# Kernel tuning notes

Measured on AMD Instinct MI355X. Metric: run time of the kernel, lower is better.

The kernel has to match this reference:

```python
import jax, jax.numpy as jnp
import numpy as np

B, T, C = 4, 2048, 1024
H, DH = 16, 64  # num_heads, head_size; H*DH == C


def setup_inputs() -> dict:
    key = jax.random.key(0)
    ks = jax.random.split(key, 6)
    s = C ** -0.5
    x = jax.random.normal(ks[0], (B, T, C), dtype=jnp.float32)
    # per-head projection weights, stacked: [H, C, DH]
    Wq = jax.random.normal(ks[1], (H, C, DH), dtype=jnp.float32) * s
    Wk = jax.random.normal(ks[2], (H, C, DH), dtype=jnp.float32) * s
    Wv = jax.random.normal(ks[3], (H, C, DH), dtype=jnp.float32) * s
    # output projection (with bias, as nn.Linear default)
    Wo = jax.random.normal(ks[4], (C, C), dtype=jnp.float32) * s
    bo = jax.random.normal(ks[5], (C,), dtype=jnp.float32) * 0.01
    return {"x": x, "Wq": Wq, "Wk": Wk, "Wv": Wv, "Wo": Wo, "bo": bo}


def reference(x, Wq, Wk, Wv, Wo, bo):
    Bv, Tv, Cv = x.shape
    scale = DH ** -0.5
    # project to per-head q/k/v: [B, H, T, DH]
    q = jnp.einsum('btc,hcd->bhtd', x, Wq)
    k = jnp.einsum('btc,hcd->bhtd', x, Wk)
    v = jnp.einsum('btc,hcd->bhtd', x, Wv)
    # scaled scores [B, H, T, T] with causal mask
    scores = jnp.einsum('bhtd,bhsd->bhts', q, k) * scale
    causal = jnp.tril(jnp.ones((Tv, Tv), dtype=bool))
    scores = jnp.where(causal, scores, -jnp.inf)
    wei = jax.nn.softmax(scores, axis=-1)
    out = jnp.einsum('bhts,bhsd->bhtd', wei, v)
    # concat heads: [B, T, H*DH] == [B, T, C]
    out = out.transpose(0, 2, 1, 3).reshape(Bv, Tv, Cv)
    return out @ Wo.T + bo
```

## Files before the change

kernel.cpp:

```cpp
#include <hip/hip_runtime.h>
#include <stdint.h>

typedef unsigned short u16;
typedef __attribute__((ext_vector_type(8))) short short8;
typedef __attribute__((ext_vector_type(4))) float floatx4;

#define MFMA_BF16 __builtin_amdgcn_mfma_f32_16x16x32_bf16

#define BB 4
#define TT 2048
#define CC 1024
#define HH 16
#define DH 64
#define MM (BB * TT)
#define NQKV (3 * CC)

#define SOFTMAX_OFF 23.083120654223414f

__device__ __forceinline__ u16 f2bf(float f) {
  union { float f; uint32_t u; } un;
  un.f = f;
  uint32_t u = un.u;
  u += 0x7fffu + ((u >> 16) & 1u);
  return (u16)(u >> 16);
}

__device__ __forceinline__ uint32_t pk2(float a, float b) {
  return (uint32_t)f2bf(a) | ((uint32_t)f2bf(b) << 16);
}

__device__ __forceinline__ void gload_lds16(const u16* g, u16* l) {
  __builtin_amdgcn_global_load_lds(
      (const __attribute__((address_space(1))) unsigned int*)g,
      (__attribute__((address_space(3))) unsigned int*)l, 16, 0, 0);
}

__global__ __launch_bounds__(256) void convert_kernel(
    const float* __restrict__ x, const float* __restrict__ Wq,
    const float* __restrict__ Wk, const float* __restrict__ Wv,
    const float* __restrict__ Wo, u16* __restrict__ xb,
    u16* __restrict__ Wt, u16* __restrict__ Wob) {
  __shared__ float T[32][33];
  int bid = blockIdx.x, tid = threadIdx.x;
  if (bid < 8192) {
    int i = (bid * 256 + tid) * 4;
    float4 f = *(const float4*)(x + i);
    uint2 o = {pk2(f.x, f.y), pk2(f.z, f.w)};
    *(uint2*)(xb + i) = o;
  } else if (bid < 8192 + 3072) {
    int tb = bid - 8192;
    int sec = tb >> 10, rem = tb & 1023;
    int h = rem >> 6, sub = rem & 63, ct = sub >> 1, dt = sub & 1;
    const float* W = (sec == 0) ? Wq : (sec == 1) ? Wk : Wv;
    int tx = tid & 31, ty = tid >> 5;
#pragma unroll
    for (int p = 0; p < 4; ++p)
      T[ty + 8 * p][tx] =
          W[((size_t)h * CC + ct * 32 + ty + 8 * p) * DH + dt * 32 + tx];
    __syncthreads();
#pragma unroll
    for (int p = 0; p < 4; ++p) {
      int n = sec * 1024 + h * 64 + dt * 32 + ty + 8 * p;
      Wt[(size_t)n * CC + ct * 32 + tx] = f2bf(T[tx][ty + 8 * p]);
    }
  } else {
    int i = ((bid - 11264) * 256 + tid) * 4;
    float4 f = *(const float4*)(Wo + i);
    uint2 o = {pk2(f.x, f.y), pk2(f.z, f.w)};
    *(uint2*)(Wob + i) = o;
  }
}

template <int MODE>
__global__ __launch_bounds__(256) void gemm_bt(
    const u16* __restrict__ A, const u16* __restrict__ Bt, int M, int N, int K,
    u16* __restrict__ qout, u16* __restrict__ kout, u16* __restrict__ vout,
    float* __restrict__ out, const float* __restrict__ bias) {
  __shared__ u16 As[128][64];
  __shared__ u16 Bs[128][64];
  int tid = threadIdx.x;
  int lane = tid & 63, w = tid >> 6;
  int wm = w >> 1, wn = w & 1;
  int g = lane >> 4, c = lane & 15;
  int m0 = blockIdx.y * 128, n0 = blockIdx.x * 128;

  floatx4 acc[4][4];
#pragma unroll
  for (int i = 0; i < 4; ++i)
#pragma unroll
    for (int j = 0; j < 4; ++j) acc[i][j] = (floatx4){0.f, 0.f, 0.f, 0.f};

  int srow = 32 * w + (lane >> 3);
  int scol = (lane & 7) * 8;
  const u16* Ag = A + (size_t)(m0 + srow) * K + scol;
  const u16* Bg = Bt + (size_t)(n0 + srow) * K + scol;
  u16* AsB = &As[32 * w][0];
  u16* BsB = &Bs[32 * w][0];

  for (int k0 = 0; k0 < K; k0 += 64) {
    __syncthreads();
#pragma unroll
    for (int j = 0; j < 4; ++j)
      gload_lds16(Ag + k0 + (size_t)j * 8 * K, AsB + j * 512);
#pragma unroll
    for (int j = 0; j < 4; ++j)
      gload_lds16(Bg + k0 + (size_t)j * 8 * K, BsB + j * 512);
    __syncthreads();
#pragma unroll
    for (int kc = 0; kc < 2; ++kc) {
      short8 af[4], bfv[4];
#pragma unroll
      for (int mt = 0; mt < 4; ++mt)
        af[mt] = *(const short8*)(&As[wm * 64 + mt * 16 + c][kc * 32 + g * 8]);
#pragma unroll
      for (int nt = 0; nt < 4; ++nt)
        bfv[nt] = *(const short8*)(&Bs[wn * 64 + nt * 16 + c][kc * 32 + g * 8]);
#pragma unroll
      for (int mt = 0; mt < 4; ++mt)
#pragma unroll
        for (int nt = 0; nt < 4; ++nt)
          acc[mt][nt] = MFMA_BF16(af[mt], bfv[nt], acc[mt][nt], 0, 0, 0);
    }
  }

#pragma unroll
  for (int mt = 0; mt < 4; ++mt) {
#pragma unroll
    for (int nt = 0; nt < 4; ++nt) {
#pragma unroll
      for (int r = 0; r < 4; ++r) {
        int m = m0 + wm * 64 + mt * 16 + g * 4 + r;
        int n = n0 + wn * 64 + nt * 16 + c;
        float v = acc[mt][nt][r];
        if (MODE == 0) {
          int b = m >> 11, t = m & 2047;
          int sec = n >> 10, h = (n >> 6) & 15, d = n & 63;
          size_t idx = (((size_t)(b * HH + h)) * TT + t) * DH + d;
          if (sec == 0)
            qout[idx] = f2bf(v * 0.18033688011112042f);
          else if (sec == 1)
            kout[idx] = f2bf(v);
          else
            vout[idx] = f2bf(v);
        } else {
          out[(size_t)m * N + n] = v + bias[n];
        }
      }
    }
  }
}

__global__ __launch_bounds__(256, 4) void flash_attn(
    const u16* __restrict__ q, const u16* __restrict__ k,
    const u16* __restrict__ v, u16* __restrict__ O) {
  __shared__ u16 Ks[64][72];
  __shared__ u16 Vs[64][72];
  __shared__ u16 Ps[4][32][72];

  int tid = threadIdx.x;
  int lane = tid & 63, w = tid >> 6;
  int g = lane >> 4, c = lane & 15;

  int id = blockIdx.y * 16 + blockIdx.x;
  int bh = id >> 4;
  int x = id & 15;
  int t0 = (((id >> 8) & 1) ? x : 15 - x) * 128;

  const u16* qb = q + (size_t)bh * TT * DH;
  const u16* kb = k + (size_t)bh * TT * DH;
  const u16* vb = v + (size_t)bh * TT * DH;

  short8 qf[2][2];
#pragma unroll
  for (int mt = 0; mt < 2; ++mt) {
    int qrow = t0 + w * 32 + mt * 16 + c;
#pragma unroll
    for (int kc = 0; kc < 2; ++kc)
      qf[mt][kc] = *(const short8*)(qb + (size_t)qrow * DH + kc * 32 + g * 8);
  }

  floatx4 oacc[2][4];
#pragma unroll
  for (int mt = 0; mt < 2; ++mt)
#pragma unroll
    for (int nt = 0; nt < 4; ++nt) oacc[mt][nt] = (floatx4){0.f, 0.f, 0.f, 0.f};
  float lsum[2][4];
#pragma unroll
  for (int mt = 0; mt < 2; ++mt)
#pragma unroll
    for (int r = 0; r < 4; ++r) lsum[mt][r] = 0.f;

  int srow = tid >> 2, scol = (tid & 3) * 16;
  const u16* kbase = kb + (size_t)srow * DH + scol;
  const u16* vbase = vb + (size_t)srow * DH + scol;

  uint4 kr0 = *(const uint4*)(kbase);
  uint4 kr1 = *(const uint4*)(kbase + 8);
  uint4 vr0 = *(const uint4*)(vbase);
  uint4 vr1 = *(const uint4*)(vbase + 8);

  int niter = (t0 >> 6) + 2;
  int nfull = t0 >> 6;
  int wmax = t0 + w * 32 + 31;
  for (int it = 0; it < niter; ++it) {
    int s0 = it << 6;
    __syncthreads();
    *(uint4*)(&Ks[srow][scol]) = kr0;
    *(uint4*)(&Ks[srow][scol + 8]) = kr1;
    {
      const u16* pv0 = (const u16*)&vr0;
      const u16* pv1 = (const u16*)&vr1;
#pragma unroll
      for (int j = 0; j < 8; ++j) {
        Vs[scol + j][srow] = pv0[j];
        Vs[scol + 8 + j][srow] = pv1[j];
      }
    }
    __syncthreads();
    if (it + 1 < niter) {
      size_t off = (size_t)((it + 1) << 6) * DH;
      kr0 = *(const uint4*)(kbase + off);
      kr1 = *(const uint4*)(kbase + off + 8);
      vr0 = *(const uint4*)(vbase + off);
      vr1 = *(const uint4*)(vbase + off + 8);
    }
    if (s0 > wmax) continue;
    bool masked = (it >= nfull);

    floatx4 z[2][4];
#pragma unroll
    for (int mt = 0; mt < 2; ++mt)
#pragma unroll
      for (int n = 0; n < 4; ++n) z[mt][n] = (floatx4){0.f, 0.f, 0.f, 0.f};
#pragma unroll
    for (int kc = 0; kc < 2; ++kc)
#pragma unroll
      for (int n = 0; n < 4; ++n) {
        short8 kf = *(const short8*)(&Ks[n * 16 + c][kc * 32 + g * 8]);
        z[0][n] = MFMA_BF16(qf[0][kc], kf, z[0][n], 0, 0, 0);
        z[1][n] = MFMA_BF16(qf[1][kc], kf, z[1][n], 0, 0, 0);
      }

#pragma unroll
    for (int mt = 0; mt < 2; ++mt) {
      int qr = t0 + w * 32 + mt * 16 + g * 4;
#pragma unroll
      for (int r = 0; r < 4; ++r) {
        float p0 = exp2f(z[mt][0][r] - SOFTMAX_OFF);
        float p1 = exp2f(z[mt][1][r] - SOFTMAX_OFF);
        float p2 = exp2f(z[mt][2][r] - SOFTMAX_OFF);
        float p3 = exp2f(z[mt][3][r] - SOFTMAX_OFF);
        if (masked) {
          if (s0 + c > qr + r) p0 = 0.f;
          if (s0 + 16 + c > qr + r) p1 = 0.f;
          if (s0 + 32 + c > qr + r) p2 = 0.f;
          if (s0 + 48 + c > qr + r) p3 = 0.f;
        }
        lsum[mt][r] += (p0 + p1) + (p2 + p3);
        u16* pr = &Ps[w][mt * 16 + g * 4 + r][c];
        pr[0] = f2bf(p0);
        pr[16] = f2bf(p1);
        pr[32] = f2bf(p2);
        pr[48] = f2bf(p3);
      }
    }

#pragma unroll
    for (int kc = 0; kc < 2; ++kc) {
      short8 pf0 = *(const short8*)(&Ps[w][c][kc * 32 + g * 8]);
      short8 pf1 = *(const short8*)(&Ps[w][16 + c][kc * 32 + g * 8]);
#pragma unroll
      for (int nt = 0; nt < 4; ++nt) {
        short8 vf = *(const short8*)(&Vs[nt * 16 + c][kc * 32 + g * 8]);
        oacc[0][nt] = MFMA_BF16(pf0, vf, oacc[0][nt], 0, 0, 0);
        oacc[1][nt] = MFMA_BF16(pf1, vf, oacc[1][nt], 0, 0, 0);
      }
    }
  }

  int b = bh >> 4, h = bh & 15;
#pragma unroll
  for (int mt = 0; mt < 2; ++mt) {
#pragma unroll
    for (int r = 0; r < 4; ++r) {
      float l = lsum[mt][r];
      l += __shfl_xor(l, 1);
      l += __shfl_xor(l, 2);
      l += __shfl_xor(l, 4);
      l += __shfl_xor(l, 8);
      lsum[mt][r] = 1.f / l;
    }
#pragma unroll
    for (int nt = 0; nt < 4; ++nt)
#pragma unroll
      for (int r = 0; r < 4; ++r) {
        int trow = t0 + w * 32 + mt * 16 + g * 4 + r;
        float ov = oacc[mt][nt][r] * lsum[mt][r];
        O[((size_t)b * TT + trow) * CC + h * DH + nt * 16 + c] = f2bf(ov);
      }
  }
}

extern "C" void kernel_launch(void* const* d_in, const int* in_sizes, int n_in,
                              void* d_out, int out_size, void* d_ws,
                              size_t ws_size, hipStream_t stream) {
  const float* x = (const float*)d_in[0];
  const float* Wq = (const float*)d_in[1];
  const float* Wk = (const float*)d_in[2];
  const float* Wv = (const float*)d_in[3];
  const float* Wo = (const float*)d_in[4];
  const float* bo = (const float*)d_in[5];
  float* out = (float*)d_out;

  u16* ws = (u16*)d_ws;
  u16* xb = ws;
  u16* Wt = xb + 8388608;
  u16* Wob = Wt + 3145728;
  u16* qw = Wob + 1048576;
  u16* kw = qw + 8388608;
  u16* vw = kw + 8388608;
  u16* Ow = xb;

  convert_kernel<<<12288, 256, 0, stream>>>(x, Wq, Wk, Wv, Wo, xb, Wt, Wob);

  gemm_bt<0><<<dim3(NQKV / 128, MM / 128), 256, 0, stream>>>(
      xb, Wt, MM, NQKV, CC, qw, kw, vw, nullptr, nullptr);

  flash_attn<<<dim3(TT / 128, BB * HH), 256, 0, stream>>>(qw, kw, vw, Ow);

  gemm_bt<1><<<dim3(CC / 128, MM / 128), 256, 0, stream>>>(
      Ow, Wob, MM, CC, CC, nullptr, nullptr, nullptr, out, bo);
}
```

Baseline: 322.8 us.

## Pre-transpose V into permuted key-major layout and vectorize P stores

Adds a separate kernel that transposes V into a [bh][d][t] layout with the keys in each 64-block permuted, so flash attention can fill its V tile with 16-byte stores instead of scalar transposing writes. The P tile is written as packed truncated bf16 in 8-byte stores using a matching column permutation, which replaces round-to-nearest with truncation. This removes LDS bank-conflicted scalar stores in the inner loop, at the cost of an extra kernel launch, an extra pass over V in global memory, more workspace, and slightly lower rounding accuracy for P.

```diff
diff --git a/kernel.cpp b/kernel.cpp
--- a/kernel.cpp
+++ b/kernel.cpp
@@ -27,6 +27,12 @@
 
 __device__ __forceinline__ uint32_t pk2(float a, float b) {
   return (uint32_t)f2bf(a) | ((uint32_t)f2bf(b) << 16);
+}
+
+__device__ __forceinline__ uint32_t pktrunc(float a, float b) {
+  union { float f; uint32_t u; } ua, ub;
+  ua.f = a; ub.f = b;
+  return __builtin_amdgcn_perm(ub.u, ua.u, 0x07060302u);
 }
 
 __device__ __forceinline__ void gload_lds16(const u16* g, u16* l) {
@@ -150,9 +156,31 @@
   }
 }
 
+__global__ __launch_bounds__(256) void vtrans(const u16* __restrict__ v,
+                                              u16* __restrict__ vP) {
+  __shared__ u16 Ld[64][72];
+  int tile = blockIdx.x, bh = blockIdx.y, tid = threadIdx.x;
+  int row = tid >> 2, col = (tid & 3) * 16;
+  const u16* src = v + ((size_t)bh * TT + tile * 64 + row) * DH + col;
+  *(uint4*)(&Ld[row][col]) = *(const uint4*)(src);
+  *(uint4*)(&Ld[row][col + 8]) = *(const uint4*)(src + 8);
+  __syncthreads();
+  int d = tid >> 2, u0 = (tid & 3) * 16;
+  union { u16 h[16]; uint4 q[2]; } o;
+#pragma unroll
+  for (int k = 0; k < 16; ++k) {
+    int u = u0 + k;
+    int s = ((u & 3) << 4) | (u >> 2);
+    o.h[k] = Ld[s][d];
+  }
+  u16* dst = vP + ((size_t)(bh * DH + d)) * TT + tile * 64 + u0;
+  *(uint4*)(dst) = o.q[0];
+  *(uint4*)(dst + 8) = o.q[1];
+}
+
 __global__ __launch_bounds__(256, 4) void flash_attn(
     const u16* __restrict__ q, const u16* __restrict__ k,
-    const u16* __restrict__ v, u16* __restrict__ O) {
+    const u16* __restrict__ vP, u16* __restrict__ O) {
   __shared__ u16 Ks[64][72];
   __shared__ u16 Vs[64][72];
   __shared__ u16 Ps[4][32][72];
@@ -168,7 +196,7 @@
 
   const u16* qb = q + (size_t)bh * TT * DH;
   const u16* kb = k + (size_t)bh * TT * DH;
-  const u16* vb = v + (size_t)bh * TT * DH;
+  const u16* vb = vP + (size_t)bh * DH * TT;
 
   short8 qf[2][2];
 #pragma unroll
@@ -192,7 +220,7 @@
 
   int srow = tid >> 2, scol = (tid & 3) * 16;
   const u16* kbase = kb + (size_t)srow * DH + scol;
-  const u16* vbase = vb + (size_t)srow * DH + scol;
+  const u16* vbase = vb + (size_t)srow * TT + scol;
 
   uint4 kr0 = *(const uint4*)(kbase);
   uint4 kr1 = *(const uint4*)(kbase + 8);
@@ -207,22 +235,16 @@
     __syncthreads();
     *(uint4*)(&Ks[srow][scol]) = kr0;
     *(uint4*)(&Ks[srow][scol + 8]) = kr1;
-    {
-      const u16* pv0 = (const u16*)&vr0;
-      const u16* pv1 = (const u16*)&vr1;
-#pragma unroll
-      for (int j = 0; j < 8; ++j) {
-        Vs[scol + j][srow] = pv0[j];
-        Vs[scol + 8 + j][srow] = pv1[j];
-      }
-    }
+    *(uint4*)(&Vs[srow][scol]) = vr0;
+    *(uint4*)(&Vs[srow][scol + 8]) = vr1;
     __syncthreads();
     if (it + 1 < niter) {
-      size_t off = (size_t)((it + 1) << 6) * DH;
-      kr0 = *(const uint4*)(kbase + off);
-      kr1 = *(const uint4*)(kbase + off + 8);
-      vr0 = *(const uint4*)(vbase + off);
-      vr1 = *(const uint4*)(vbase + off + 8);
+      size_t koff = (size_t)((it + 1) << 6) * DH;
+      int voff = (it + 1) << 6;
+      kr0 = *(const uint4*)(kbase + koff);
+      kr1 = *(const uint4*)(kbase + koff + 8);
+      vr0 = *(const uint4*)(vbase + voff);
+      vr1 = *(const uint4*)(vbase + voff + 8);
     }
     if (s0 > wmax) continue;
     bool masked = (it >= nfull);
@@ -257,11 +279,8 @@
           if (s0 + 48 + c > qr + r) p3 = 0.f;
         }
         lsum[mt][r] += (p0 + p1) + (p2 + p3);
-        u16* pr = &Ps[w][mt * 16 + g * 4 + r][c];
-        pr[0] = f2bf(p0);
-        pr[16] = f2bf(p1);
-        pr[32] = f2bf(p2);
-        pr[48] = f2bf(p3);
+        uint2 pk = {pktrunc(p0, p1), pktrunc(p2, p3)};
+        *(uint2*)(&Ps[w][mt * 16 + g * 4 + r][4 * c]) = pk;
       }
     }
 
@@ -319,6 +338,7 @@
   u16* qw = Wob + 1048576;
   u16* kw = qw + 8388608;
   u16* vw = kw + 8388608;
+  u16* vP = vw + 8388608;
   u16* Ow = xb;
 
   convert_kernel<<<12288, 256, 0, stream>>>(x, Wq, Wk, Wv, Wo, xb, Wt, Wob);
@@ -326,7 +346,9 @@
   gemm_bt<0><<<dim3(NQKV / 128, MM / 128), 256, 0, stream>>>(
       xb, Wt, MM, NQKV, CC, qw, kw, vw, nullptr, nullptr);
 
-  flash_attn<<<dim3(TT / 128, BB * HH), 256, 0, stream>>>(qw, kw, vw, Ow);
+  vtrans<<<dim3(TT / 64, BB * HH), 256, 0, stream>>>(vw, vP);
+
+  flash_attn<<<dim3(TT / 128, BB * HH), 256, 0, stream>>>(qw, kw, vP, Ow);
 
   gemm_bt<1><<<dim3(CC / 128, MM / 128), 256, 0, stream>>>(
       Ow, Wob, MM, CC, CC, nullptr, nullptr, nullptr, out, bo);
```

Result: faster. 314.2 us (-2.7%).
